# Performance work log

Hardware: AMD Instinct MI355X
Metric: run time of the kernel (lower is better)

## Reference

```python
import jax, jax.numpy as jnp
import numpy as np

SEQ_LEN, BATCH, INPUT_SIZE, LATENT, N_CLASS = 512, 256, 512, 1024, 1000


def setup_inputs() -> dict:
    key = jax.random.key(0)
    k_x, k_w, k_b, k_wc, k_bc = jax.random.split(key, 5)
    scale_cell = 1.0 / np.sqrt(INPUT_SIZE + LATENT)
    scale_cls = 1.0 / np.sqrt(LATENT)
    return {
        "x": jax.random.normal(k_x, (SEQ_LEN, BATCH, INPUT_SIZE), dtype=jnp.float32),
        # nn.Linear(input_size+latent, latent): weight [latent, input_size+latent]
        "W": jax.random.uniform(k_w, (LATENT, INPUT_SIZE + LATENT), dtype=jnp.float32, minval=-scale_cell, maxval=scale_cell),
        "b": jax.random.uniform(k_b, (LATENT,), dtype=jnp.float32, minval=-scale_cell, maxval=scale_cell),
        # nn.Linear(latent, n_class): weight [n_class, latent]
        "Wc": jax.random.uniform(k_wc, (N_CLASS, LATENT), dtype=jnp.float32, minval=-scale_cls, maxval=scale_cls),
        "bc": jax.random.uniform(k_bc, (N_CLASS,), dtype=jnp.float32, minval=-scale_cls, maxval=scale_cls),
    }


def reference(x, W, b, Wc, bc):
    # x: [L, B, D]; tanh-RNN scan over L, then classify final hidden state.
    latent = W.shape[0]
    h0 = jnp.zeros((x.shape[1], latent), dtype=x.dtype)

    def step(h, xt):
        # concat([x_t, h]) @ W^T + b, then tanh  -> new hidden [B, latent]
        h_new = jnp.tanh(jnp.concatenate([xt, h], axis=-1) @ W.T + b)
        return h_new, None

    h_final, _ = jax.lax.scan(step, h0, x)
    return h_final @ Wc.T + bc  # [B, n_class]
```

## Files before the change

### kernel.cpp

```cpp
#include <hip/hip_runtime.h>

typedef _Float16 f16;
typedef _Float16 f16x8 __attribute__((ext_vector_type(8)));
typedef float f32x4 __attribute__((ext_vector_type(4)));
typedef float f32x16 __attribute__((ext_vector_type(16)));
typedef unsigned int u32;
typedef u32 u32x4 __attribute__((ext_vector_type(4)));

#define SEQ 512
#define BATCH 256
#define DIN 512
#define DH 1024
#define DK 1536
#define NCLS 1000

#define NGROUP 8
#define ROWS 32
#define OUTS 32
#define KSLICES 96
#define RED_STRIDE 33

#define SMEM_ALLOC (96 * 1024)

#define POLL_GUARD 8192

#define XLDS1_OFF 32768
#define RED_OFF3  65536
#define RED_BYTES (4 * OUTS * RED_STRIDE * 4)
#define BLDS_OFF  (RED_OFF3 + RED_BYTES)
#define META_OFF  (BLDS_OFF + OUTS * 4)

#define WF_OFF     0
#define HP_OFF     ((size_t)4 << 20)
#define HP_GROUP   65536
#define HP_HALF    ((size_t)NGROUP * HP_GROUP)
#define HP_BYTES   (2 * HP_HALF)
#define SLOT_OFF   ((size_t)6 << 20)
#define SLOT_BYTES (NGROUP * 64)
#define XF_OFF     ((size_t)8 << 20)
#define XF_BYTES   ((size_t)SEQ * NGROUP * 32 * 1024)
#define WS_NEED    (XF_OFF + XF_BYTES)

#define TAGBITS 0x40004000u
#define STRIPM  0xBFFFBFFFu

__device__ __forceinline__ u32x4 hload4(const void* p) {
    u32x4 v;
    asm volatile("global_load_dwordx4 %0, %1, off sc0" : "=v"(v) : "v"(p) : "memory");
    return v;
}
__device__ __forceinline__ void hstore8(void* p, uint2 v) {
    asm volatile("global_store_dwordx2 %0, %1, off sc0" :: "v"(p), "v"(v) : "memory");
}
__device__ __forceinline__ void glds16(const void* gsrc, void* ldst) {
    __builtin_amdgcn_global_load_lds(
        (const __attribute__((address_space(1))) u32*)gsrc,
        (__attribute__((address_space(3))) u32*)ldst, 16, 0, 0);
}
__device__ __forceinline__ void barrier_lgkm_only() {
    __builtin_amdgcn_sched_barrier(0);
    asm volatile("s_waitcnt lgkmcnt(0)" ::: "memory");
    __builtin_amdgcn_s_barrier();
    asm volatile("" ::: "memory");
    __builtin_amdgcn_sched_barrier(0);
}

__global__ void __launch_bounds__(256) convert_W_kernel(const float* __restrict__ W,
                                                        f16* __restrict__ Wf) {
    int id = blockIdx.x * 256 + threadIdx.x;
    if (id >= DH * DK) return;
    int v = id & 7;
    int l = (id >> 3) & 63;
    int rest = id >> 9;
    int j = rest % KSLICES;
    int s = rest / KSLICES;
    int row = s * OUTS + (l & 31);
    int k = j * 16 + ((l >> 5) << 3) + v;
    Wf[id] = (f16)W[row * DK + k];
}

__global__ void __launch_bounds__(256) convert_x_kernel(const float* __restrict__ x,
                                                        f16* __restrict__ xf) {
    __shared__ f16 tile[ROWS * DIN];
    const int tid = threadIdx.x;
    const float* src = x + (size_t)blockIdx.x * (ROWS * DIN);
#pragma unroll
    for (int c = 0; c < 16; ++c) {
        int off = (c * 256 + tid) * 4;
        f32x4 a = *(const f32x4*)(src + off);
        union { f16 h[4]; uint2 u; } uu;
        uu.h[0] = (f16)a[0]; uu.h[1] = (f16)a[1]; uu.h[2] = (f16)a[2]; uu.h[3] = (f16)a[3];
        *(uint2*)&tile[off] = uu.u;
    }
    __syncthreads();
    char* dst = (char*)xf + (size_t)blockIdx.x * 32768 + tid * 128;
    int j = tid >> 3;
    int l0 = (tid & 7) * 8;
    f16x8 buf[8];
#pragma unroll
    for (int e = 0; e < 8; ++e) {
        int l = l0 + e;
        buf[e] = *(const f16x8*)&tile[(l & 31) * DIN + j * 16 + (l >> 5) * 8];
    }
#pragma unroll
    for (int e = 0; e < 8; ++e) *(f16x8*)(dst + e * 16) = buf[e];
}

template<bool XF>
__global__ void __launch_bounds__(256, 1)
rnn_kernel(const float* __restrict__ x, const float* __restrict__ bias,
           const f16* __restrict__ Wf, const f16* __restrict__ xf,
           f16* __restrict__ hpack, int* __restrict__ xslots) {
    extern __shared__ char smem[];
    char*  xlds = smem;
    float* red  = (float*)(smem + RED_OFF3);
    float* blds = (float*)(smem + BLDS_OFF);
    int*   meta = (int*)(smem + META_OFF);

    const int tid  = threadIdx.x;
    const int wave = tid >> 6;
    const int lane = tid & 63;
    const int r    = lane & 31;
    const int hi   = lane >> 5;

    if (tid == 0) {
        u32 xcc;
        asm volatile("s_getreg_b32 %0, hwreg(HW_REG_XCC_ID)" : "=s"(xcc));
        meta[0] = (int)(xcc & 7);
        meta[1] = atomicAdd(&xslots[xcc & 7], 1) & 31;
    }
    __syncthreads();
    const int g = meta[0];
    const int s = meta[1];
    if (tid < OUTS) blds[tid] = bias[s * OUTS + tid];

    f16x8 wf[24];
    {
        const f16x8* wp = ((const f16x8*)Wf) + (size_t)s * KSLICES * 64 + lane;
#pragma unroll
        for (int i = 0; i < 24; ++i) wf[i] = wp[(size_t)(wave + 4 * i) * 64];
    }

    const int b_ = tid >> 3, o0 = (tid & 7) * 4;
    const int fj = (s << 1) + (o0 >> 4);
    const size_t foff = (size_t)fj * 1024 + ((((o0 >> 3) & 1) << 5) + b_) * 16 + (o0 & 7) * 2;

    const int srow = tid >> 6, scol = (tid & 63) * 8;
    const int sj = scol >> 4, shi = (scol >> 3) & 1, sswz = (sj & 7) << 4;

    union cvt_t { u32x4 u; f16x8 h; };

    if constexpr (XF) {
        const char* xg = (const char*)xf + (size_t)g * 32768 + lane * 16;
#pragma unroll
        for (int i = 0; i < 8; ++i) {
            int j = wave + 4 * i;
            glds16(xg + j * 1024, xlds + j * 1024);
        }
        asm volatile("s_waitcnt vmcnt(0)" ::: "memory");
        __syncthreads();
    }

    for (int t = 0; t < SEQ; ++t) {
        if constexpr (!XF) {
            const float* xt = x + ((size_t)t * BATCH + g * ROWS) * DIN;
#pragma unroll
            for (int i = 0; i < 8; ++i) {
                int row = srow + 4 * i;
                const float* xp = xt + row * DIN + scol;
                f32x4 a0 = *(const f32x4*)xp;
                f32x4 a1 = *(const f32x4*)(xp + 4);
                f16x8 o;
                o[0] = (f16)a0[0]; o[1] = (f16)a0[1]; o[2] = (f16)a0[2]; o[3] = (f16)a0[3];
                o[4] = (f16)a1[0]; o[5] = (f16)a1[1]; o[6] = (f16)a1[2]; o[7] = (f16)a1[3];
                *(f16x8*)(xlds + ((sj * 1024 + ((shi << 5) + row) * 16) ^ sswz)) = o;
            }
            __syncthreads();
        }

        f32x16 accA = {0,0,0,0, 0,0,0,0, 0,0,0,0, 0,0,0,0};
        f32x16 accB = {0,0,0,0, 0,0,0,0, 0,0,0,0, 0,0,0,0};

        {
            const char* xc = xlds + (XF ? (t & 1) * XLDS1_OFF : 0);
#pragma unroll
            for (int i = 0; i < 8; ++i) {
                int j = wave + 4 * i;
                f16x8 bf;
                if constexpr (XF)
                    bf = *(const f16x8*)(xc + j * 1024 + lane * 16);
                else
                    bf = *(const f16x8*)(xc + ((j * 1024 + lane * 16) ^ ((j & 7) << 4)));
                if (i & 1) accB = __builtin_amdgcn_mfma_f32_32x32x16_f16(wf[i], bf, accB, 0, 0, 0);
                else       accA = __builtin_amdgcn_mfma_f32_32x32x16_f16(wf[i], bf, accA, 0, 0, 0);
            }
        }

        if constexpr (XF) {
            int tn = t + 1; if (tn == SEQ) tn = SEQ - 1;
            const char* xg = (const char*)xf + (size_t)(tn * NGROUP + g) * 32768 + lane * 16;
            char* xn = xlds + ((t + 1) & 1) * XLDS1_OFF;
#pragma unroll
            for (int i = 0; i < 8; ++i) {
                int j = wave + 4 * i;
                glds16(xg + j * 1024, xn + j * 1024);
            }
        }

        {
            const char* hpb = (const char*)hpack + (size_t)((t & 1) * NGROUP + g) * HP_GROUP
                            + wave * 1024 + lane * 16;
            const u32 rtag = (u32)((t >> 1) & 1);
#pragma unroll
            for (int hh = 0; hh < 2; ++hh) {
                const char* pb = hpb + hh * 32768;
                u32x4 hv[8];
                int guard = POLL_GUARD;
                if (rtag == 0) {
                    for (;;) {
#pragma unroll
                        for (int q = 0; q < 8; ++q) hv[q] = hload4(pb + q * 4096);
                        asm volatile("s_waitcnt vmcnt(0)" ::: "memory");
                        __builtin_amdgcn_sched_barrier(0);
                        u32 orr = 0;
#pragma unroll
                        for (int q = 0; q < 8; ++q) orr |= hv[q].x | hv[q].y | hv[q].z | hv[q].w;
                        if (__all((orr & TAGBITS) == 0u)) break;
                        if (--guard == 0) break;
                    }
                } else {
                    for (;;) {
#pragma unroll
                        for (int q = 0; q < 8; ++q) hv[q] = hload4(pb + q * 4096);
                        asm volatile("s_waitcnt vmcnt(0)" ::: "memory");
                        __builtin_amdgcn_sched_barrier(0);
                        u32 andv = 0xFFFFFFFFu;
#pragma unroll
                        for (int q = 0; q < 8; ++q) andv &= hv[q].x & hv[q].y & hv[q].z & hv[q].w;
                        if (__all((andv & TAGBITS) == TAGBITS)) break;
                        if (--guard == 0) break;
                    }
#pragma unroll
                    for (int q = 0; q < 8; ++q) hv[q] &= STRIPM;
                }
                __builtin_amdgcn_sched_barrier(0);
#pragma unroll
                for (int q = 0; q < 8; ++q) {
                    cvt_t c; c.u = hv[q];
                    if (q & 1) accB = __builtin_amdgcn_mfma_f32_32x32x16_f16(wf[8 + 8 * hh + q], c.h, accB, 0, 0, 0);
                    else       accA = __builtin_amdgcn_mfma_f32_32x32x16_f16(wf[8 + 8 * hh + q], c.h, accA, 0, 0, 0);
                }
            }
        }

        {
            float* rw = red + wave * (OUTS * RED_STRIDE);
            int rb = hi << 2;
#pragma unroll
            for (int v = 0; v < 16; ++v) {
                int orow = (v & 3) + 8 * (v >> 2) + rb;
                rw[orow * RED_STRIDE + r] = accA[v] + accB[v];
            }
        }
        if constexpr (XF) barrier_lgkm_only();
        else              __syncthreads();

        {
            const u32 wtag = (u32)(((t + 1) >> 1) & 1);
            char* hob = (char*)hpack + (size_t)(((t + 1) & 1) * NGROUP + g) * HP_GROUP + foff;
            union { f16 h4[4]; uint2 u; } uu;
#pragma unroll
            for (int i = 0; i < 4; ++i) {
                int o = o0 + i;
                float p = blds[o];
#pragma unroll
                for (int w2 = 0; w2 < 4; ++w2)
                    p += red[w2 * (OUTS * RED_STRIDE) + o * RED_STRIDE + b_];
                float e = __expf(2.f * p);
                uu.h4[i] = (f16)(1.f - 2.f / (e + 1.f));
            }
            if (wtag) { uu.u.x |= TAGBITS; uu.u.y |= TAGBITS; }
            hstore8(hob, uu.u);
        }
        if constexpr (XF) barrier_lgkm_only();
    }
}

__global__ void __launch_bounds__(256) classify_kernel(const f16* __restrict__ hpack,
                                                       const float* __restrict__ Wc,
                                                       const float* __restrict__ bc,
                                                       float* __restrict__ out) {
    __shared__ float wrow[DH];
    int c = blockIdx.x;
    int tid = threadIdx.x;
    for (int i = tid; i < DH; i += 256) wrow[i] = Wc[(size_t)c * DH + i];
    __syncthreads();
    int g = tid >> 5, r2 = tid & 31;
    const char* base = (const char*)hpack + (size_t)g * HP_GROUP;
    float acc = bc[c];
    for (int j = 0; j < 64; ++j) {
#pragma unroll
        for (int h2 = 0; h2 < 2; ++h2) {
            f16x8 hv = *(const f16x8*)(base + j * 1024 + ((h2 << 5) + r2) * 16);
            int k = j * 16 + h2 * 8;
#pragma unroll
            for (int v = 0; v < 8; ++v) acc += (float)hv[v] * wrow[k + v];
        }
    }
    out[(size_t)tid * NCLS + c] = acc;
}

extern "C" void kernel_launch(void* const* d_in, const int* in_sizes, int n_in,
                              void* d_out, int out_size, void* d_ws, size_t ws_size,
                              hipStream_t stream) {
    const float* x  = (const float*)d_in[0];
    const float* W  = (const float*)d_in[1];
    const float* b  = (const float*)d_in[2];
    const float* Wc = (const float*)d_in[3];
    const float* bc = (const float*)d_in[4];
    float* out = (float*)d_out;

    char* ws = (char*)d_ws;
    f16* Wf     = (f16*)(ws + WF_OFF);
    f16* hpack  = (f16*)(ws + HP_OFF);
    int* xslots = (int*)(ws + SLOT_OFF);
    f16* xf     = (f16*)(ws + XF_OFF);

    const bool bigws = (ws_size >= WS_NEED);

    hipMemsetAsync(hpack, 0, HP_HALF, stream);
    hipMemsetAsync((char*)hpack + HP_HALF, 0x40, HP_HALF, stream);
    hipMemsetAsync(xslots, 0, SLOT_BYTES, stream);

    convert_W_kernel<<<(DH * DK + 255) / 256, 256, 0, stream>>>(W, Wf);
    if (bigws)
        convert_x_kernel<<<dim3(SEQ * NGROUP), dim3(256), 0, stream>>>(x, xf);

    const void* kfn = bigws ? (const void*)rnn_kernel<true>
                            : (const void*)rnn_kernel<false>;
    hipFuncSetAttribute(kfn, hipFuncAttributeMaxDynamicSharedMemorySize, SMEM_ALLOC);
    void* args[6];
    args[0] = (void*)&x;
    args[1] = (void*)&b;
    args[2] = (void*)&Wf;
    args[3] = (void*)&xf;
    args[4] = (void*)&hpack;
    args[5] = (void*)&xslots;
    hipLaunchCooperativeKernel(kfn, dim3(256), dim3(256), args, SMEM_ALLOC, stream);

    classify_kernel<<<dim3(NCLS), dim3(256), 0, stream>>>(hpack, Wc, bc, out);
}
```

Before: 1.260 ms.

## Replace tag-bit polling on hidden state with per-block step flags

```diff
diff --git a/kernel.cpp b/kernel.cpp
--- a/kernel.cpp
+++ b/kernel.cpp
@@ -22,7 +22,8 @@
 
 #define SMEM_ALLOC (96 * 1024)
 
-#define POLL_GUARD 8192
+#define POLL_GUARD  8192
+#define FLAG_GUARD  (1 << 17)
 
 #define XLDS1_OFF 32768
 #define RED_OFF3  65536
@@ -35,7 +36,9 @@
 #define HP_GROUP   65536
 #define HP_HALF    ((size_t)NGROUP * HP_GROUP)
 #define HP_BYTES   (2 * HP_HALF)
-#define SLOT_OFF   ((size_t)6 << 20)
+#define FLG_OFF    ((size_t)6 << 20)
+#define FLG_BYTES  (NGROUP * 32 * 128)
+#define SLOT_OFF   (FLG_OFF + 65536)
 #define SLOT_BYTES (NGROUP * 64)
 #define XF_OFF     ((size_t)8 << 20)
 #define XF_BYTES   ((size_t)SEQ * NGROUP * 32 * 1024)
@@ -51,6 +54,15 @@
 }
 __device__ __forceinline__ void hstore8(void* p, uint2 v) {
     asm volatile("global_store_dwordx2 %0, %1, off sc0" :: "v"(p), "v"(v) : "memory");
+}
+__device__ __forceinline__ u32 flag_poll_load(const u32* p) {
+    u32 v;
+    asm volatile("global_load_dword %0, %1, off sc0\n\ts_waitcnt vmcnt(0)"
+                 : "=v"(v) : "v"(p) : "memory");
+    return v;
+}
+__device__ __forceinline__ void flag_store(u32* p, u32 v) {
+    asm volatile("global_store_dword %0, %1, off sc0" :: "v"(p), "v"(v) : "memory");
 }
 __device__ __forceinline__ void glds16(const void* gsrc, void* ldst) {
     __builtin_amdgcn_global_load_lds(
@@ -110,7 +122,8 @@
 __global__ void __launch_bounds__(256, 1)
 rnn_kernel(const float* __restrict__ x, const float* __restrict__ bias,
            const f16* __restrict__ Wf, const f16* __restrict__ xf,
-           f16* __restrict__ hpack, int* __restrict__ xslots) {
+           f16* __restrict__ hpack, u32* __restrict__ flags,
+           int* __restrict__ xslots) {
     extern __shared__ char smem[];
     char*  xlds = smem;
     float* red  = (float*)(smem + RED_OFF3);
@@ -140,6 +153,9 @@
 #pragma unroll
         for (int i = 0; i < 24; ++i) wf[i] = wp[(size_t)(wave + 4 * i) * 64];
     }
+
+    const u32* fpoll = flags + ((size_t)g * 32 + (lane >> 1)) * 32;
+    u32* fmine = flags + ((size_t)g * 32 + s) * 32;
 
     const int b_ = tid >> 3, o0 = (tid & 7) * 4;
     const int fj = (s << 1) + (o0 >> 4);
@@ -181,6 +197,8 @@
         f32x16 accA = {0,0,0,0, 0,0,0,0, 0,0,0,0, 0,0,0,0};
         f32x16 accB = {0,0,0,0, 0,0,0,0, 0,0,0,0, 0,0,0,0};
 
+        if constexpr (XF) { asm volatile("s_waitcnt vmcnt(0)" ::: "memory");
+                            __builtin_amdgcn_sched_barrier(0); }
         {
             const char* xc = xlds + (XF ? (t & 1) * XLDS1_OFF : 0);
 #pragma unroll
@@ -207,7 +225,42 @@
             }
         }
 
-        {
+        if constexpr (XF) {
+            if (wave == 0) {
+                int guard = FLAG_GUARD;
+                for (;;) {
+                    u32 v = flag_poll_load(fpoll);
+                    if (__all(v >= (u32)t)) break;
+                    if (--guard == 0) break;
+                    __builtin_amdgcn_s_sleep(1);
+                }
+            }
+            __syncthreads();
+
+            const char* hpb = (const char*)hpack + (size_t)((t & 1) * NGROUP + g) * HP_GROUP
+                            + wave * 1024 + lane * 16;
+            u32x4 hvA[8], hvB[8];
+#pragma unroll
+            for (int q = 0; q < 8; ++q) hvA[q] = hload4(hpb + q * 4096);
+#pragma unroll
+            for (int q = 0; q < 8; ++q) hvB[q] = hload4(hpb + 32768 + q * 4096);
+            asm volatile("s_waitcnt vmcnt(8)" ::: "memory");
+            __builtin_amdgcn_sched_barrier(0);
+#pragma unroll
+            for (int q = 0; q < 8; ++q) {
+                cvt_t c; c.u = hvA[q];
+                if (q & 1) accB = __builtin_amdgcn_mfma_f32_32x32x16_f16(wf[8 + q], c.h, accB, 0, 0, 0);
+                else       accA = __builtin_amdgcn_mfma_f32_32x32x16_f16(wf[8 + q], c.h, accA, 0, 0, 0);
+            }
+            asm volatile("s_waitcnt vmcnt(0)" ::: "memory");
+            __builtin_amdgcn_sched_barrier(0);
+#pragma unroll
+            for (int q = 0; q < 8; ++q) {
+                cvt_t c; c.u = hvB[q];
+                if (q & 1) accB = __builtin_amdgcn_mfma_f32_32x32x16_f16(wf[16 + q], c.h, accB, 0, 0, 0);
+                else       accA = __builtin_amdgcn_mfma_f32_32x32x16_f16(wf[16 + q], c.h, accA, 0, 0, 0);
+            }
+        } else {
             const char* hpb = (const char*)hpack + (size_t)((t & 1) * NGROUP + g) * HP_GROUP
                             + wave * 1024 + lane * 16;
             const u32 rtag = (u32)((t >> 1) & 1);
@@ -266,7 +319,6 @@
         else              __syncthreads();
 
         {
-            const u32 wtag = (u32)(((t + 1) >> 1) & 1);
             char* hob = (char*)hpack + (size_t)(((t + 1) & 1) * NGROUP + g) * HP_GROUP + foff;
             union { f16 h4[4]; uint2 u; } uu;
 #pragma unroll
@@ -279,10 +331,21 @@
                 float e = __expf(2.f * p);
                 uu.h4[i] = (f16)(1.f - 2.f / (e + 1.f));
             }
-            if (wtag) { uu.u.x |= TAGBITS; uu.u.y |= TAGBITS; }
-            hstore8(hob, uu.u);
-        }
-        if constexpr (XF) barrier_lgkm_only();
+            if constexpr (XF) {
+                hstore8(hob, uu.u);
+            } else {
+                const u32 wtag = (u32)(((t + 1) >> 1) & 1);
+                if (wtag) { uu.u.x |= TAGBITS; uu.u.y |= TAGBITS; }
+                hstore8(hob, uu.u);
+            }
+        }
+
+        if constexpr (XF) {
+            __syncthreads();
+            if (tid == 0) flag_store(fmine, (u32)(t + 1));
+        } else {
+            barrier_lgkm_only();
+        }
     }
 }
 
@@ -323,6 +386,7 @@
     char* ws = (char*)d_ws;
     f16* Wf     = (f16*)(ws + WF_OFF);
     f16* hpack  = (f16*)(ws + HP_OFF);
+    u32* flags  = (u32*)(ws + FLG_OFF);
     int* xslots = (int*)(ws + SLOT_OFF);
     f16* xf     = (f16*)(ws + XF_OFF);
 
@@ -330,6 +394,7 @@
 
     hipMemsetAsync(hpack, 0, HP_HALF, stream);
     hipMemsetAsync((char*)hpack + HP_HALF, 0x40, HP_HALF, stream);
+    hipMemsetAsync(flags, 0, FLG_BYTES, stream);
     hipMemsetAsync(xslots, 0, SLOT_BYTES, stream);
 
     convert_W_kernel<<<(DH * DK + 255) / 256, 256, 0, stream>>>(W, Wf);
@@ -339,13 +404,14 @@
     const void* kfn = bigws ? (const void*)rnn_kernel<true>
                             : (const void*)rnn_kernel<false>;
     hipFuncSetAttribute(kfn, hipFuncAttributeMaxDynamicSharedMemorySize, SMEM_ALLOC);
-    void* args[6];
+    void* args[7];
     args[0] = (void*)&x;
     args[1] = (void*)&b;
     args[2] = (void*)&Wf;
     args[3] = (void*)&xf;
     args[4] = (void*)&hpack;
-    args[5] = (void*)&xslots;
+    args[5] = (void*)&flags;
+    args[6] = (void*)&xslots;
     hipLaunchCooperativeKernel(kfn, dim3(256), dim3(256), args, SMEM_ALLOC, stream);
 
     classify_kernel<<<dim3(NCLS), dim3(256), 0, stream>>>(hpack, Wc, bc, out);
```

Measured after the change: 1.331 ms. 1.06x slower.
